# Performance work log

Measured on AMD Instinct MI355X. Metric: run time of the kernel, lower is better.

Reference implementation:

```python
import jax, jax.numpy as jnp
import numpy as np

B, M, FIN, OUT, K = 64, 512, 128, 128, 2
SLOPE = 0.01  # F.leaky_relu default negative_slope


def setup_inputs() -> dict:
    key = jax.random.key(0)
    k0, k1, k2, k3 = jax.random.split(key, 4)
    x = jax.random.normal(k0, (B, M, FIN), jnp.float32)
    La = jax.random.normal(k1, (B, M, M), jnp.float32)
    weight = jax.random.normal(k2, (FIN * K, OUT), jnp.float32) * np.sqrt(2.0 / (FIN * K + OUT))
    bias = jnp.zeros((OUT,), jnp.float32)
    M_L = jax.random.normal(k3, (FIN, FIN), jnp.float32) * np.sqrt(2.0 / FIN)
    return {"x": x, "La": La, "weight": weight, "bias": bias, "M_L": M_L}


def _leaky(v):
    return jnp.where(v >= 0, v, SLOPE * v)


def _per_mol(xm, Lm, weight, bias, M_L):
    # xm: [M, FIN], Lm: [M, M]
    # compute_laplacian: pairwise Euclidean distances of x @ M_L via gram trick
    xw = xm @ M_L                                   # [M, FIN]
    sq = jnp.sum(xw * xw, axis=-1)                  # [M]
    d2 = sq[:, None] + sq[None, :] - 2.0 * (xw @ xw.T)
    dist = jnp.sqrt(jnp.maximum(d2, 1e-12))         # safe sqrt (diag is 0)
    W = jnp.exp(-dist)                              # [M, M]
    d = W.sum(axis=1) + 1e-7
    dis = 1.0 / jnp.sqrt(d)
    L = jnp.eye(M, dtype=xm.dtype) - dis[:, None] * W * dis[None, :]
    # clip_by_average_norm(clip_norm=1)
    avg_norm = jnp.linalg.norm(L) / (M * M)
    factor = jnp.minimum(1.0 / (avg_norm + 1e-6), 1.0)
    res_L = _leaky(L * factor)
    L_all = res_L + Lm
    # Chebyshev recursion (K terms)
    xs = [xm]
    if K > 1:
        xs.append(L_all @ xm)
    for _ in range(2, K):
        xs.append(2.0 * (L_all @ xs[-1]) - xs[-2])
    xk = jnp.stack(xs, axis=0)                      # [K, M, FIN]
    xk = jnp.transpose(xk, (1, 2, 0)).reshape(M, K * FIN)  # matches permute(1,2,0).view
    out = _leaky(xk @ weight + bias)                # activation 'relu' maps to leaky_relu
    return out, res_L, W


def reference(x, La, weight, bias, M_L):
    out, L_upd, W_upd = jax.vmap(lambda xm, Lm: _per_mol(xm, Lm, weight, bias, M_L))(x, La)
    return out, L_upd, W_upd
```

## Files before the change

### kernel.cpp

```cpp
#include <hip/hip_runtime.h>


#define BB 64
#define MM 512
#define FINC 128
#define OUTC 128

typedef short bf16x8 __attribute__((ext_vector_type(8)));
typedef float f32x4 __attribute__((ext_vector_type(4)));

__device__ __forceinline__ float leaky_(float v) { return v >= 0.0f ? v : 0.01f * v; }
__device__ __forceinline__ unsigned short f2bf(float f) {
    unsigned int u = __float_as_uint(f);
    return (unsigned short)((u + 0x7FFF + ((u >> 16) & 1)) >> 16);
}

__global__ __launch_bounds__(256) void k_xw(const float* __restrict__ x,
                                            const float* __restrict__ ml,
                                            unsigned short* __restrict__ xwb,
                                            float* __restrict__ sq,
                                            unsigned short* __restrict__ xTb) {
    const int b = blockIdx.y, i0 = blockIdx.x * 64;
    const int tid = threadIdx.x, ty4 = (tid >> 4) * 4, tx4 = (tid & 15) * 4;
    __shared__ float a_t[64][129];
    __shared__ float b_t[64][129];
    __shared__ float red[64][17];

    const float* xb = x + ((size_t)b * MM + i0) * FINC;
#pragma unroll
    for (int q = 0; q < 8; ++q) {
        int idx4 = tid + q * 256;
        int r = idx4 >> 5, k4 = (idx4 & 31) * 4;
        float4 v = *(const float4*)(xb + r * FINC + k4);
        a_t[r][k4 + 0] = v.x; a_t[r][k4 + 1] = v.y;
        a_t[r][k4 + 2] = v.z; a_t[r][k4 + 3] = v.w;
    }

    float acc[4][8];
#pragma unroll
    for (int m = 0; m < 4; ++m)
#pragma unroll
        for (int n = 0; n < 8; ++n) acc[m][n] = 0.0f;

    for (int kc = 0; kc < 2; ++kc) {
        __syncthreads();
#pragma unroll
        for (int q = 0; q < 8; ++q) {
            int idx4 = tid + q * 256;
            int kk = idx4 >> 5, c4 = (idx4 & 31) * 4;
            float4 v = *(const float4*)(ml + (size_t)(kc * 64 + kk) * FINC + c4);
            b_t[kk][c4 + 0] = v.x; b_t[kk][c4 + 1] = v.y;
            b_t[kk][c4 + 2] = v.z; b_t[kk][c4 + 3] = v.w;
        }
        __syncthreads();
#pragma unroll 4
        for (int k = 0; k < 64; ++k) {
            float av[4], bv[8];
#pragma unroll
            for (int m = 0; m < 4; ++m) av[m] = a_t[ty4 + m][kc * 64 + k];
#pragma unroll
            for (int n = 0; n < 4; ++n) { bv[n] = b_t[k][tx4 + n]; bv[4 + n] = b_t[k][64 + tx4 + n]; }
#pragma unroll
            for (int m = 0; m < 4; ++m)
#pragma unroll
                for (int n = 0; n < 8; ++n) acc[m][n] = fmaf(av[m], bv[n], acc[m][n]);
        }
    }

    unsigned short* xwbb = xwb + ((size_t)b * MM + i0) * FINC;
#pragma unroll
    for (int m = 0; m < 4; ++m) {
        ushort4 h0, h1;
        h0.x = f2bf(acc[m][0]); h0.y = f2bf(acc[m][1]); h0.z = f2bf(acc[m][2]); h0.w = f2bf(acc[m][3]);
        h1.x = f2bf(acc[m][4]); h1.y = f2bf(acc[m][5]); h1.z = f2bf(acc[m][6]); h1.w = f2bf(acc[m][7]);
        *(ushort4*)(xwbb + (ty4 + m) * FINC + tx4) = h0;
        *(ushort4*)(xwbb + (ty4 + m) * FINC + 64 + tx4) = h1;
        float p = 0.0f;
#pragma unroll
        for (int n = 0; n < 8; ++n) p = fmaf(acc[m][n], acc[m][n], p);
        red[ty4 + m][tid & 15] = p;
    }
    __syncthreads();
    if (tid < 64) {
        float s = 0.0f;
#pragma unroll
        for (int t = 0; t < 16; ++t) s += red[tid][t];
        sq[b * MM + i0 + tid] = s;
    }
#pragma unroll
    for (int q = 0; q < 16; ++q) {
        int idx = tid + q * 256;
        int c = idx >> 5, j2 = (idx & 31) * 2;
        ushort2 t;
        t.x = f2bf(a_t[j2][c]);
        t.y = f2bf(a_t[j2 + 1][c]);
        *(ushort2*)(xTb + ((size_t)b * FINC + c) * MM + i0 + j2) = t;
    }
}

__global__ __launch_bounds__(256) void k_gram(const unsigned short* __restrict__ xwb,
                                              const float* __restrict__ sq,
                                              float* __restrict__ Wout,
                                              float* __restrict__ dis) {
    const int b = blockIdx.y, i0 = blockIdx.x * 64;
    const int tid = threadIdx.x;
    const int w = tid >> 6, l = tid & 63, lr = l & 15, lg = l >> 4;
    const unsigned short* xb = xwb + (size_t)b * MM * FINC;
    const int ia = i0 + w * 16 + lr;
    const unsigned short* arow = xb + (size_t)ia * FINC + lg * 8;
    bf16x8 a0 = *(const bf16x8*)(arow + 0);
    bf16x8 a1 = *(const bf16x8*)(arow + 32);
    bf16x8 a2 = *(const bf16x8*)(arow + 64);
    bf16x8 a3 = *(const bf16x8*)(arow + 96);

    const int id0 = i0 + w * 16 + lg * 4;
    const float* sqb = sq + b * MM;
    const float si0 = sqb[id0 + 0], si1 = sqb[id0 + 1], si2 = sqb[id0 + 2], si3 = sqb[id0 + 3];
    float rs0 = 0.f, rs1 = 0.f, rs2 = 0.f, rs3 = 0.f;
    float* Wb = Wout + (size_t)b * MM * MM;

    const unsigned short* jr0 = xb + (size_t)lr * FINC + lg * 8;
    bf16x8 c0 = *(const bf16x8*)(jr0 + 0);
    bf16x8 c1 = *(const bf16x8*)(jr0 + 32);
    bf16x8 c2 = *(const bf16x8*)(jr0 + 64);
    bf16x8 c3 = *(const bf16x8*)(jr0 + 96);
    float sjc = sqb[lr];

#pragma unroll
    for (int tl = 0; tl < 32; ++tl) {
        const int nt = (tl < 31) ? tl + 1 : 31;
        const unsigned short* nr = xb + (size_t)(nt * 16 + lr) * FINC + lg * 8;
        bf16x8 n0 = *(const bf16x8*)(nr + 0);
        bf16x8 n1 = *(const bf16x8*)(nr + 32);
        bf16x8 n2 = *(const bf16x8*)(nr + 64);
        bf16x8 n3 = *(const bf16x8*)(nr + 96);
        float sjn = sqb[nt * 16 + lr];

        f32x4 acc = {0.f, 0.f, 0.f, 0.f};
        acc = __builtin_amdgcn_mfma_f32_16x16x32_bf16(a0, c0, acc, 0, 0, 0);
        acc = __builtin_amdgcn_mfma_f32_16x16x32_bf16(a1, c1, acc, 0, 0, 0);
        acc = __builtin_amdgcn_mfma_f32_16x16x32_bf16(a2, c2, acc, 0, 0, 0);
        acc = __builtin_amdgcn_mfma_f32_16x16x32_bf16(a3, c3, acc, 0, 0, 0);

        const int jc = tl * 16 + lr;
        float d2, wv;
        d2 = si0 + sjc - 2.f * acc[0]; if (id0 + 0 == jc) d2 = 0.f;
        wv = __expf(-sqrtf(fmaxf(d2, 1e-12f)));
        Wb[(size_t)(id0 + 0) * MM + jc] = wv; rs0 += wv;
        d2 = si1 + sjc - 2.f * acc[1]; if (id0 + 1 == jc) d2 = 0.f;
        wv = __expf(-sqrtf(fmaxf(d2, 1e-12f)));
        Wb[(size_t)(id0 + 1) * MM + jc] = wv; rs1 += wv;
        d2 = si2 + sjc - 2.f * acc[2]; if (id0 + 2 == jc) d2 = 0.f;
        wv = __expf(-sqrtf(fmaxf(d2, 1e-12f)));
        Wb[(size_t)(id0 + 2) * MM + jc] = wv; rs2 += wv;
        d2 = si3 + sjc - 2.f * acc[3]; if (id0 + 3 == jc) d2 = 0.f;
        wv = __expf(-sqrtf(fmaxf(d2, 1e-12f)));
        Wb[(size_t)(id0 + 3) * MM + jc] = wv; rs3 += wv;

        c0 = n0; c1 = n1; c2 = n2; c3 = n3; sjc = sjn;
    }
#pragma unroll
    for (int msk = 1; msk < 16; msk <<= 1) {
        rs0 += __shfl_xor(rs0, msk);
        rs1 += __shfl_xor(rs1, msk);
        rs2 += __shfl_xor(rs2, msk);
        rs3 += __shfl_xor(rs3, msk);
    }
    if (lr == 0) {
        dis[b * MM + id0 + 0] = 1.0f / sqrtf(rs0 + 1e-7f);
        dis[b * MM + id0 + 1] = 1.0f / sqrtf(rs1 + 1e-7f);
        dis[b * MM + id0 + 2] = 1.0f / sqrtf(rs2 + 1e-7f);
        dis[b * MM + id0 + 3] = 1.0f / sqrtf(rs3 + 1e-7f);
    }
}

__global__ __launch_bounds__(256) void k_fuse(const float* __restrict__ Wout,
                                              const float* __restrict__ La,
                                              const unsigned short* __restrict__ xTb,
                                              const float* __restrict__ dis,
                                              const float* __restrict__ x,
                                              const float* __restrict__ weight,
                                              const float* __restrict__ bias,
                                              float* __restrict__ resL,
                                              float* __restrict__ out) {
    const int b = blockIdx.y, i0 = blockIdx.x * 64;
    const int tid = threadIdx.x;
    const int w = tid >> 6, l = tid & 63, lr = l & 15, lg = l >> 4;
    const int ia = i0 + w * 16 + lr;
    const float* disb = dis + b * MM;
    const float di = disb[ia];
    const float* Wr = Wout + (size_t)b * MM * MM + (size_t)ia * MM;
    const float* Lr = La   + (size_t)b * MM * MM + (size_t)ia * MM;
    float* Rr = resL + (size_t)b * MM * MM + (size_t)ia * MM;
    const unsigned short* xTm = xTb + (size_t)b * FINC * MM;

    __shared__ unsigned short y_lds[64][136];

    f32x4 acc[8];
#pragma unroll
    for (int n = 0; n < 8; ++n) acc[n] = (f32x4){0.f, 0.f, 0.f, 0.f};

#define LD2(W0, W1, L0, L1, t) { const int kk_ = (t) * 32 + lg * 8; \
    W0 = *(const float4*)(Wr + kk_); W1 = *(const float4*)(Wr + kk_ + 4); \
    L0 = *(const float4*)(Lr + kk_); L1 = *(const float4*)(Lr + kk_ + 4); }

#define STEP(CW0, CW1, CL0, CL1, t) { \
    const int koff = (t) * 32 + lg * 8; \
    bf16x8 bfr[8]; \
    _Pragma("unroll") \
    for (int n = 0; n < 8; ++n) \
        bfr[n] = *(const bf16x8*)(xTm + (size_t)(n * 16 + lr) * MM + koff); \
    float4 dj0 = *(const float4*)(disb + koff); \
    float4 dj1 = *(const float4*)(disb + koff + 4); \
    const int dd = ia - koff; \
    const float* wp0 = &CW0.x; const float* wp1 = &CW1.x; \
    const float* lp0 = &CL0.x; const float* lp1 = &CL1.x; \
    const float* dp0 = &dj0.x; const float* dp1 = &dj1.x; \
    float4 r0, r1; float* rp0 = &r0.x; float* rp1 = &r1.x; \
    bf16x8 af; \
    _Pragma("unroll") \
    for (int e = 0; e < 4; ++e) { \
        float Lv = ((dd == e) ? 1.0f : 0.0f) - di * wp0[e] * dp0[e]; \
        float rv = leaky_(Lv);                \
        rp0[e] = rv; \
        af[e] = (short)f2bf(rv + lp0[e]); \
    } \
    _Pragma("unroll") \
    for (int e = 0; e < 4; ++e) { \
        float Lv = ((dd == e + 4) ? 1.0f : 0.0f) - di * wp1[e] * dp1[e]; \
        float rv = leaky_(Lv); \
        rp1[e] = rv; \
        af[e + 4] = (short)f2bf(rv + lp1[e]); \
    } \
    *(float4*)(Rr + koff) = r0; \
    *(float4*)(Rr + koff + 4) = r1; \
    _Pragma("unroll") \
    for (int n = 0; n < 8; ++n) \
        acc[n] = __builtin_amdgcn_mfma_f32_16x16x32_bf16(af, bfr[n], acc[n], 0, 0, 0); \
}

    float4 aw0, aw1, al0, al1, bw0, bw1, bl0, bl1, tw0, tw1, tl0, tl1;
    LD2(aw0, aw1, al0, al1, 0);
    LD2(bw0, bw1, bl0, bl1, 1);
#pragma unroll
    for (int tp = 0; tp < 8; ++tp) {
        const int t0 = tp * 2, t1 = tp * 2 + 1;
        if (t0 + 2 < 16) { LD2(tw0, tw1, tl0, tl1, t0 + 2); }
        STEP(aw0, aw1, al0, al1, t0);
        if (t0 + 2 < 16) { aw0 = tw0; aw1 = tw1; al0 = tl0; al1 = tl1; }
        if (t1 + 2 < 16) { LD2(tw0, tw1, tl0, tl1, t1 + 2); }
        STEP(bw0, bw1, bl0, bl1, t1);
        if (t1 + 2 < 16) { bw0 = tw0; bw1 = tw1; bl0 = tl0; bl1 = tl1; }
    }
#undef LD2
#undef STEP

    const int r0l = w * 16 + lg * 4;
#pragma unroll
    for (int n = 0; n < 8; ++n) {
        const int col = n * 16 + lr;
#pragma unroll
        for (int rg = 0; rg < 4; ++rg)
            y_lds[r0l + rg][col] = f2bf(acc[n][rg]);
    }
    __syncthreads();

    const float* xr = x + ((size_t)b * MM + ia) * FINC;
    const int yrow = w * 16 + lr;
    f32x4 acc2[8];
#pragma unroll
    for (int n = 0; n < 8; ++n) acc2[n] = (f32x4){0.f, 0.f, 0.f, 0.f};

#pragma unroll
    for (int ch = 0; ch < 8; ++ch) {
        const int koff = ch * 32 + lg * 8;
        const int f0 = koff >> 1;
        float4 xv = *(const float4*)(xr + f0);
        ushort4 yv = *(const ushort4*)&y_lds[yrow][f0];
        bf16x8 af;
        af[0] = (short)f2bf(xv.x); af[1] = (short)yv.x;
        af[2] = (short)f2bf(xv.y); af[3] = (short)yv.y;
        af[4] = (short)f2bf(xv.z); af[5] = (short)yv.z;
        af[6] = (short)f2bf(xv.w); af[7] = (short)yv.w;
#pragma unroll
        for (int n = 0; n < 8; ++n) {
            const int col = n * 16 + lr;
            bf16x8 bf;
#pragma unroll
            for (int j = 0; j < 8; ++j)
                bf[j] = (short)f2bf(weight[(size_t)(koff + j) * OUTC + col]);
            acc2[n] = __builtin_amdgcn_mfma_f32_16x16x32_bf16(af, bf, acc2[n], 0, 0, 0);
        }
    }

    const int id0 = i0 + w * 16 + lg * 4;
    float* ob = out + (size_t)b * MM * OUTC;
#pragma unroll
    for (int n = 0; n < 8; ++n) {
        const int col = n * 16 + lr;
        const float bs = bias[col];
#pragma unroll
        for (int rg = 0; rg < 4; ++rg)
            ob[(size_t)(id0 + rg) * OUTC + col] = leaky_(acc2[n][rg] + bs);
    }
}

extern "C" void kernel_launch(void* const* d_in, const int* in_sizes, int n_in,
                              void* d_out, int out_size, void* d_ws, size_t ws_size,
                              hipStream_t stream) {
    const float* x      = (const float*)d_in[0];
    const float* La     = (const float*)d_in[1];
    const float* weight = (const float*)d_in[2];
    const float* bias   = (const float*)d_in[3];
    const float* ml     = (const float*)d_in[4];

    float* out0 = (float*)d_out;
    float* out1 = out0 + (size_t)BB * MM * OUTC;
    float* out2 = out1 + (size_t)BB * MM * MM;

    unsigned short* xwb = (unsigned short*)d_ws;
    unsigned short* xTb = xwb + 4194304;
    float* sq  = (float*)((char*)d_ws + 16777216);
    float* dis = sq + 32768;

    dim3 blk(256);
    k_xw   <<<dim3(8, BB), blk, 0, stream>>>(x, ml, xwb, sq, xTb);
    k_gram <<<dim3(8, BB), blk, 0, stream>>>(xwb, sq, out2, dis);
    k_fuse <<<dim3(8, BB), blk, 0, stream>>>(out2, La, xTb, dis, x, weight, bias, out1, out0);
}
```

Before: 317.9 us.

## Recompute gram distances in fused kernel instead of round-tripping W through memory

The gram kernel now only computes row sums to produce the normalisation factors and no longer stores W. The fused kernel recomputes the gram tile with MFMA, writes W and res_L directly, and stages the bf16 L_all tile in LDS for the Chebyshev matmul. This removes a full read of the 64 MB W matrix, in exchange for doing the gram MFMA and exp twice. Stores and loads now use scalar per-lane accesses rather than float4, which may lower memory efficiency.

```diff
diff --git a/kernel.cpp b/kernel.cpp
--- a/kernel.cpp
+++ b/kernel.cpp
@@ -98,10 +98,9 @@
     }
 }
 
-__global__ __launch_bounds__(256) void k_gram(const unsigned short* __restrict__ xwb,
-                                              const float* __restrict__ sq,
-                                              float* __restrict__ Wout,
-                                              float* __restrict__ dis) {
+__global__ __launch_bounds__(256) void k_dis(const unsigned short* __restrict__ xwb,
+                                             const float* __restrict__ sq,
+                                             float* __restrict__ dis) {
     const int b = blockIdx.y, i0 = blockIdx.x * 64;
     const int tid = threadIdx.x;
     const int w = tid >> 6, l = tid & 63, lr = l & 15, lg = l >> 4;
@@ -117,7 +116,6 @@
     const float* sqb = sq + b * MM;
     const float si0 = sqb[id0 + 0], si1 = sqb[id0 + 1], si2 = sqb[id0 + 2], si3 = sqb[id0 + 3];
     float rs0 = 0.f, rs1 = 0.f, rs2 = 0.f, rs3 = 0.f;
-    float* Wb = Wout + (size_t)b * MM * MM;
 
     const unsigned short* jr0 = xb + (size_t)lr * FINC + lg * 8;
     bf16x8 c0 = *(const bf16x8*)(jr0 + 0);
@@ -143,19 +141,15 @@
         acc = __builtin_amdgcn_mfma_f32_16x16x32_bf16(a3, c3, acc, 0, 0, 0);
 
         const int jc = tl * 16 + lr;
-        float d2, wv;
+        float d2;
         d2 = si0 + sjc - 2.f * acc[0]; if (id0 + 0 == jc) d2 = 0.f;
-        wv = __expf(-sqrtf(fmaxf(d2, 1e-12f)));
-        Wb[(size_t)(id0 + 0) * MM + jc] = wv; rs0 += wv;
+        rs0 += __expf(-sqrtf(fmaxf(d2, 1e-12f)));
         d2 = si1 + sjc - 2.f * acc[1]; if (id0 + 1 == jc) d2 = 0.f;
-        wv = __expf(-sqrtf(fmaxf(d2, 1e-12f)));
-        Wb[(size_t)(id0 + 1) * MM + jc] = wv; rs1 += wv;
+        rs1 += __expf(-sqrtf(fmaxf(d2, 1e-12f)));
         d2 = si2 + sjc - 2.f * acc[2]; if (id0 + 2 == jc) d2 = 0.f;
-        wv = __expf(-sqrtf(fmaxf(d2, 1e-12f)));
-        Wb[(size_t)(id0 + 2) * MM + jc] = wv; rs2 += wv;
+        rs2 += __expf(-sqrtf(fmaxf(d2, 1e-12f)));
         d2 = si3 + sjc - 2.f * acc[3]; if (id0 + 3 == jc) d2 = 0.f;
-        wv = __expf(-sqrtf(fmaxf(d2, 1e-12f)));
-        Wb[(size_t)(id0 + 3) * MM + jc] = wv; rs3 += wv;
+        rs3 += __expf(-sqrtf(fmaxf(d2, 1e-12f)));
 
         c0 = n0; c1 = n1; c2 = n2; c3 = n3; sjc = sjn;
     }
@@ -174,86 +168,90 @@
     }
 }
 
-__global__ __launch_bounds__(256) void k_fuse(const float* __restrict__ Wout,
+__global__ __launch_bounds__(256) void k_fuse(const unsigned short* __restrict__ xwb,
+                                              const unsigned short* __restrict__ xTb,
+                                              const float* __restrict__ sq,
+                                              const float* __restrict__ dis,
                                               const float* __restrict__ La,
-                                              const unsigned short* __restrict__ xTb,
-                                              const float* __restrict__ dis,
                                               const float* __restrict__ x,
                                               const float* __restrict__ weight,
                                               const float* __restrict__ bias,
+                                              float* __restrict__ Wout,
                                               float* __restrict__ resL,
                                               float* __restrict__ out) {
     const int b = blockIdx.y, i0 = blockIdx.x * 64;
     const int tid = threadIdx.x;
     const int w = tid >> 6, l = tid & 63, lr = l & 15, lg = l >> 4;
     const int ia = i0 + w * 16 + lr;
+    const int id0 = i0 + w * 16 + lg * 4;
+
+    const unsigned short* xb = xwb + (size_t)b * MM * FINC;
+    const unsigned short* xTm = xTb + (size_t)b * FINC * MM;
+    const float* sqb = sq + b * MM;
     const float* disb = dis + b * MM;
-    const float di = disb[ia];
-    const float* Wr = Wout + (size_t)b * MM * MM + (size_t)ia * MM;
-    const float* Lr = La   + (size_t)b * MM * MM + (size_t)ia * MM;
-    float* Rr = resL + (size_t)b * MM * MM + (size_t)ia * MM;
-    const unsigned short* xTm = xTb + (size_t)b * FINC * MM;
-
-    __shared__ unsigned short y_lds[64][136];
+    float* Wb = Wout + (size_t)b * MM * MM;
+    float* Rb = resL + (size_t)b * MM * MM;
+    const float* Lab = La + (size_t)b * MM * MM;
+
+    __shared__ unsigned short LT[64][136];
+
+    const unsigned short* arow = xb + (size_t)ia * FINC + lg * 8;
+    bf16x8 a0 = *(const bf16x8*)(arow + 0);
+    bf16x8 a1 = *(const bf16x8*)(arow + 32);
+    bf16x8 a2 = *(const bf16x8*)(arow + 64);
+    bf16x8 a3 = *(const bf16x8*)(arow + 96);
+
+    float si[4], dsi[4];
+#pragma unroll
+    for (int r = 0; r < 4; ++r) { si[r] = sqb[id0 + r]; dsi[r] = disb[id0 + r]; }
 
     f32x4 acc[8];
 #pragma unroll
     for (int n = 0; n < 8; ++n) acc[n] = (f32x4){0.f, 0.f, 0.f, 0.f};
 
-#define LD2(W0, W1, L0, L1, t) { const int kk_ = (t) * 32 + lg * 8; \
-    W0 = *(const float4*)(Wr + kk_); W1 = *(const float4*)(Wr + kk_ + 4); \
-    L0 = *(const float4*)(Lr + kk_); L1 = *(const float4*)(Lr + kk_ + 4); }
-
-#define STEP(CW0, CW1, CL0, CL1, t) { \
-    const int koff = (t) * 32 + lg * 8; \
-    bf16x8 bfr[8]; \
-    _Pragma("unroll") \
-    for (int n = 0; n < 8; ++n) \
-        bfr[n] = *(const bf16x8*)(xTm + (size_t)(n * 16 + lr) * MM + koff); \
-    float4 dj0 = *(const float4*)(disb + koff); \
-    float4 dj1 = *(const float4*)(disb + koff + 4); \
-    const int dd = ia - koff; \
-    const float* wp0 = &CW0.x; const float* wp1 = &CW1.x; \
-    const float* lp0 = &CL0.x; const float* lp1 = &CL1.x; \
-    const float* dp0 = &dj0.x; const float* dp1 = &dj1.x; \
-    float4 r0, r1; float* rp0 = &r0.x; float* rp1 = &r1.x; \
-    bf16x8 af; \
-    _Pragma("unroll") \
-    for (int e = 0; e < 4; ++e) { \
-        float Lv = ((dd == e) ? 1.0f : 0.0f) - di * wp0[e] * dp0[e]; \
-        float rv = leaky_(Lv);                \
-        rp0[e] = rv; \
-        af[e] = (short)f2bf(rv + lp0[e]); \
-    } \
-    _Pragma("unroll") \
-    for (int e = 0; e < 4; ++e) { \
-        float Lv = ((dd == e + 4) ? 1.0f : 0.0f) - di * wp1[e] * dp1[e]; \
-        float rv = leaky_(Lv); \
-        rp1[e] = rv; \
-        af[e + 4] = (short)f2bf(rv + lp1[e]); \
-    } \
-    *(float4*)(Rr + koff) = r0; \
-    *(float4*)(Rr + koff + 4) = r1; \
-    _Pragma("unroll") \
-    for (int n = 0; n < 8; ++n) \
-        acc[n] = __builtin_amdgcn_mfma_f32_16x16x32_bf16(af, bfr[n], acc[n], 0, 0, 0); \
-}
-
-    float4 aw0, aw1, al0, al1, bw0, bw1, bl0, bl1, tw0, tw1, tl0, tl1;
-    LD2(aw0, aw1, al0, al1, 0);
-    LD2(bw0, bw1, bl0, bl1, 1);
-#pragma unroll
-    for (int tp = 0; tp < 8; ++tp) {
-        const int t0 = tp * 2, t1 = tp * 2 + 1;
-        if (t0 + 2 < 16) { LD2(tw0, tw1, tl0, tl1, t0 + 2); }
-        STEP(aw0, aw1, al0, al1, t0);
-        if (t0 + 2 < 16) { aw0 = tw0; aw1 = tw1; al0 = tl0; al1 = tl1; }
-        if (t1 + 2 < 16) { LD2(tw0, tw1, tl0, tl1, t1 + 2); }
-        STEP(bw0, bw1, bl0, bl1, t1);
-        if (t1 + 2 < 16) { bw0 = tw0; bw1 = tw1; bl0 = tl0; bl1 = tl1; }
-    }
-#undef LD2
-#undef STEP
+    for (int ch = 0; ch < 4; ++ch) {
+        const int jbase = ch * 128;
+#pragma unroll
+        for (int n8 = 0; n8 < 8; ++n8) {
+            const int jc = jbase + n8 * 16 + lr;
+            const unsigned short* jrow = xb + (size_t)jc * FINC + lg * 8;
+            bf16x8 b0 = *(const bf16x8*)(jrow + 0);
+            bf16x8 b1 = *(const bf16x8*)(jrow + 32);
+            bf16x8 b2 = *(const bf16x8*)(jrow + 64);
+            bf16x8 b3 = *(const bf16x8*)(jrow + 96);
+            f32x4 g = {0.f, 0.f, 0.f, 0.f};
+            g = __builtin_amdgcn_mfma_f32_16x16x32_bf16(a0, b0, g, 0, 0, 0);
+            g = __builtin_amdgcn_mfma_f32_16x16x32_bf16(a1, b1, g, 0, 0, 0);
+            g = __builtin_amdgcn_mfma_f32_16x16x32_bf16(a2, b2, g, 0, 0, 0);
+            g = __builtin_amdgcn_mfma_f32_16x16x32_bf16(a3, b3, g, 0, 0, 0);
+            const float sj = sqb[jc];
+            const float dj = disb[jc];
+#pragma unroll
+            for (int r = 0; r < 4; ++r) {
+                const int gi = id0 + r;
+                float d2 = si[r] + sj - 2.f * g[r];
+                const bool dg = (gi == jc);
+                if (dg) d2 = 0.f;
+                const float wv = __expf(-sqrtf(fmaxf(d2, 1e-12f)));
+                Wb[(size_t)gi * MM + jc] = wv;
+                const float Lv = (dg ? 1.0f : 0.0f) - dsi[r] * wv * dj;
+                const float rv = leaky_(Lv);
+                Rb[(size_t)gi * MM + jc] = rv;
+                LT[w * 16 + lg * 4 + r][n8 * 16 + lr] = f2bf(rv + Lab[(size_t)gi * MM + jc]);
+            }
+        }
+        __syncthreads();
+#pragma unroll
+        for (int kidx = 0; kidx < 4; ++kidx) {
+            bf16x8 af = *(const bf16x8*)&LT[w * 16 + lr][kidx * 32 + lg * 8];
+#pragma unroll
+            for (int n = 0; n < 8; ++n) {
+                bf16x8 bf = *(const bf16x8*)(xTm + (size_t)(n * 16 + lr) * MM + jbase + kidx * 32 + lg * 8);
+                acc[n] = __builtin_amdgcn_mfma_f32_16x16x32_bf16(af, bf, acc[n], 0, 0, 0);
+            }
+        }
+        __syncthreads();
+    }
 
     const int r0l = w * 16 + lg * 4;
 #pragma unroll
@@ -261,7 +259,7 @@
         const int col = n * 16 + lr;
 #pragma unroll
         for (int rg = 0; rg < 4; ++rg)
-            y_lds[r0l + rg][col] = f2bf(acc[n][rg]);
+            LT[r0l + rg][col] = f2bf(acc[n][rg]);
     }
     __syncthreads();
 
@@ -272,11 +270,11 @@
     for (int n = 0; n < 8; ++n) acc2[n] = (f32x4){0.f, 0.f, 0.f, 0.f};
 
 #pragma unroll
-    for (int ch = 0; ch < 8; ++ch) {
-        const int koff = ch * 32 + lg * 8;
+    for (int chp = 0; chp < 8; ++chp) {
+        const int koff = chp * 32 + lg * 8;
         const int f0 = koff >> 1;
         float4 xv = *(const float4*)(xr + f0);
-        ushort4 yv = *(const ushort4*)&y_lds[yrow][f0];
+        ushort4 yv = *(const ushort4*)&LT[yrow][f0];
         bf16x8 af;
         af[0] = (short)f2bf(xv.x); af[1] = (short)yv.x;
         af[2] = (short)f2bf(xv.y); af[3] = (short)yv.y;
@@ -293,7 +291,6 @@
         }
     }
 
-    const int id0 = i0 + w * 16 + lg * 4;
     float* ob = out + (size_t)b * MM * OUTC;
 #pragma unroll
     for (int n = 0; n < 8; ++n) {
@@ -325,6 +322,6 @@
 
     dim3 blk(256);
     k_xw   <<<dim3(8, BB), blk, 0, stream>>>(x, ml, xwb, sq, xTb);
-    k_gram <<<dim3(8, BB), blk, 0, stream>>>(xwb, sq, out2, dis);
-    k_fuse <<<dim3(8, BB), blk, 0, stream>>>(out2, La, xTb, dis, x, weight, bias, out1, out0);
-}
+    k_dis  <<<dim3(8, BB), blk, 0, stream>>>(xwb, sq, dis);
+    k_fuse <<<dim3(8, BB), blk, 0, stream>>>(xwb, xTb, sq, dis, La, x, weight, bias, out2, out1, out0);
+}
```

Result: slower. 347.2 us (+9.2%).
